# Performance work log

Hardware: AMD Instinct MI355X
Metric: run time of the kernel (lower is better)

Reference implementation:

```python
import jax, jax.numpy as jnp
import numpy as np

N_GRID, N_MESH, N_EDGE, H = 65536, 10242, 131072, 512

def _layernorm(x, g, b, eps=1e-5):
    m = jnp.mean(x, axis=-1, keepdims=True)
    v = jnp.var(x, axis=-1, keepdims=True)
    return (x - m) * jax.lax.rsqrt(v + eps) * g + b

def _mlp(x, W1, b1, W2, b2, g, b):
    # Linear -> SiLU -> Linear -> LayerNorm (GraphCast MeshGraphMLP)
    h = jax.nn.silu(x @ W1 + b1)
    return _layernorm(h @ W2 + b2, g, b)

def setup_inputs() -> dict:
    key = jax.random.key(0)
    ks = jax.random.split(key, 16)
    s = lambda fan_in: 1.0 / np.sqrt(fan_in)
    inp = {
        'grid_node_features': jax.random.normal(ks[0], (N_GRID, H), jnp.float32),
        'mesh_node_features': jax.random.normal(ks[1], (N_MESH, H), jnp.float32),
        'grid2mesh_edge_features': jax.random.normal(ks[2], (N_EDGE, H), jnp.float32),
        'src_indices': jax.random.randint(ks[3], (N_EDGE,), 0, N_GRID),
        'dst_indices': jax.random.randint(ks[4], (N_EDGE,), 0, N_MESH),
        # edge MLP: in = concat(edge, src, dst) = 3H
        'We1': jax.random.normal(ks[5], (3 * H, H), jnp.float32) * s(3 * H),
        'be1': jnp.zeros((H,), jnp.float32),
        'We2': jax.random.normal(ks[6], (H, H), jnp.float32) * s(H),
        'be2': jnp.zeros((H,), jnp.float32),
        'ge': jnp.ones((H,), jnp.float32), 'bbe': jnp.zeros((H,), jnp.float32),
        # node MLP: in = concat(node, agg) = 2H
        'Wn1': jax.random.normal(ks[7], (2 * H, H), jnp.float32) * s(2 * H),
        'bn1': jnp.zeros((H,), jnp.float32),
        'Wn2': jax.random.normal(ks[8], (H, H), jnp.float32) * s(H),
        'bn2': jnp.zeros((H,), jnp.float32),
        'gn': jnp.ones((H,), jnp.float32), 'bbn': jnp.zeros((H,), jnp.float32),
        # grid node MLP: H -> H
        'Wg1': jax.random.normal(ks[9], (H, H), jnp.float32) * s(H),
        'bg1': jnp.zeros((H,), jnp.float32),
        'Wg2': jax.random.normal(ks[10], (H, H), jnp.float32) * s(H),
        'bg2': jnp.zeros((H,), jnp.float32),
        'gg': jnp.ones((H,), jnp.float32), 'bbg': jnp.zeros((H,), jnp.float32),
    }
    return inp

def reference(grid_node_features, mesh_node_features, grid2mesh_edge_features,
              src_indices, dst_indices,
              We1, be1, We2, be2, ge, bbe,
              Wn1, bn1, Wn2, bn2, gn, bbn,
              Wg1, bg1, Wg2, bg2, gg, bbg):
    # --- MeshEdgeBlock: gather src/dst, concat, MLP, residual on edges ---
    cat_e = jnp.concatenate([grid2mesh_edge_features,
                             grid_node_features[src_indices],
                             mesh_node_features[dst_indices]], axis=-1)  # [E, 3H]
    e_feats = grid2mesh_edge_features + _mlp(cat_e, We1, be1, We2, be2, ge, bbe)
    # --- MeshNodeBlock: scatter-sum edges to mesh nodes, concat, MLP ---
    agg = jax.ops.segment_sum(e_feats, dst_indices, num_segments=N_MESH)  # [M, H]
    cat_n = jnp.concatenate([mesh_node_features, agg], axis=-1)  # [M, 2H]
    n_feats = _mlp(cat_n, Wn1, bn1, Wn2, bn2, gn, bbn)
    mesh_out = mesh_node_features + n_feats
    # --- grid node MLP + residual ---
    grid_out = grid_node_features + _mlp(grid_node_features, Wg1, bg1, Wg2, bg2, gg, bbg)
    return (grid_out, mesh_out)
```

## Files before the change

### kernel.cpp

```cpp
#include <hip/hip_runtime.h>
#include <stdint.h>

typedef unsigned short u16;
typedef unsigned int   u32;
typedef unsigned char  u8;

using bf16x8 = __attribute__((ext_vector_type(8))) short;
using f32x4  = __attribute__((ext_vector_type(4))) float;

#define DEVF static __device__ __forceinline__

DEVF u16 f2bf(float f){
  u32 u = __builtin_bit_cast(u32, f);
  u32 r = u + 0x7FFFu + ((u >> 16) & 1u);
  return (u16)(r >> 16);
}
DEVF float bf2f(u16 h){
  u32 u = ((u32)h) << 16;
  return __builtin_bit_cast(float, u);
}

DEVF void gload_lds16(const u16* g, u16* s){
  __builtin_amdgcn_global_load_lds(
      (const __attribute__((address_space(1))) u32*)g,
      (__attribute__((address_space(3))) u32*)(u32)(uintptr_t)s,
      16, 0, 0);
}


__global__ __launch_bounds__(256) void k_f32_to_bf16(const float* __restrict__ in,
                                                     u16* __restrict__ out, long n){
  long i = (long)blockIdx.x * blockDim.x + threadIdx.x;
  long stride = (long)gridDim.x * blockDim.x;
  for (long j = i * 8; j < n; j += stride * 8){
    float4 a = *(const float4*)(in + j);
    float4 b = *(const float4*)(in + j + 4);
    bf16x8 v;
    v[0]=(short)f2bf(a.x); v[1]=(short)f2bf(a.y); v[2]=(short)f2bf(a.z); v[3]=(short)f2bf(a.w);
    v[4]=(short)f2bf(b.x); v[5]=(short)f2bf(b.y); v[6]=(short)f2bf(b.z); v[7]=(short)f2bf(b.w);
    *(bf16x8*)(out + j) = v;
  }
}

__global__ __launch_bounds__(256)
void k_conv_perm(const float* __restrict__ in, const int* __restrict__ pos,
                 u16* __restrict__ out, int E){
  int e = blockIdx.x * 4 + (threadIdx.x >> 6);
  int l = threadIdx.x & 63;
  if (e >= E) return;
  const float* r = in + (size_t)e * 512 + l * 8;
  float4 a = *(const float4*)r, b = *(const float4*)(r + 4);
  bf16x8 v;
  v[0]=(short)f2bf(a.x); v[1]=(short)f2bf(a.y); v[2]=(short)f2bf(a.z); v[3]=(short)f2bf(a.w);
  v[4]=(short)f2bf(b.x); v[5]=(short)f2bf(b.y); v[6]=(short)f2bf(b.z); v[7]=(short)f2bf(b.w);
  *(bf16x8*)(out + (size_t)pos[e] * 512 + l * 8) = v;
}

__global__ __launch_bounds__(256) void k_zero_i32(int* __restrict__ p, int n){
  int i = blockIdx.x * 256 + threadIdx.x;
  if (i < n) p[i] = 0;
}

__global__ __launch_bounds__(256) void k_transpose_w_off(const float* __restrict__ W,
                                                         u16* __restrict__ Wt,
                                                         int K, int N, int k0){
  int idx = blockIdx.x * 256 + threadIdx.x;
  if (idx < K * N){
    int k = idx / N, n = idx - k * N;
    Wt[(size_t)n * K + k] = f2bf(W[(size_t)(k + k0) * N + n]);
  }
}


__global__ __launch_bounds__(256)
void k_hist(const int* __restrict__ key, int* __restrict__ cnt, int E){
  int e = blockIdx.x * 256 + threadIdx.x;
  if (e < E) atomicAdd(&cnt[key[e]], 1);
}

__global__ __launch_bounds__(1024)
void k_scan(const int* __restrict__ cnt, int* __restrict__ offs, int n){
  __shared__ int part[1024];
  int t = threadIdx.x;
  const int PER = (n + 1023) / 1024;
  int base = t * PER;
  int s = 0;
  for (int i = 0; i < PER; ++i){ int idx = base + i; if (idx < n) s += cnt[idx]; }
  part[t] = s;
  __syncthreads();
  for (int o = 1; o < 1024; o <<= 1){
    int v = (t >= o) ? part[t - o] : 0;
    __syncthreads();
    part[t] += v;
    __syncthreads();
  }
  int run = (t == 0) ? 0 : part[t - 1];
  for (int i = 0; i < PER; ++i){
    int idx = base + i;
    if (idx < n){ offs[idx] = run; run += cnt[idx]; }
  }
  if (t == 1023) offs[n] = part[1023];
}

__global__ __launch_bounds__(256)
void k_scatter_pos(const int* __restrict__ key, const int* __restrict__ srcIn,
                   const int* __restrict__ offs, int* __restrict__ cur,
                   int* __restrict__ pos, int* __restrict__ srcD,
                   int* __restrict__ dstD, int E){
  int e = blockIdx.x * 256 + threadIdx.x;
  if (e < E){
    int d = key[e];
    int p = offs[d] + atomicAdd(&cur[d], 1);
    pos[e] = p;
    srcD[p] = srcIn[e];
    dstD[p] = d;
  }
}


#define LDA4(BUF, MH, KK, AF) \
  _Pragma("unroll") for (int m_ = 0; m_ < 4; ++m_) \
    AF[m_] = *(const bf16x8*)&lA[BUF][(wm * 128 + (MH) * 64 + m_ * 16 + lane16) * 64 + \
                                      ((((KK) << 2) | kl) ^ (lane16 & 7)) * 8];

#define LDB4(BUF, KK, BFR) \
  _Pragma("unroll") for (int n_ = 0; n_ < 4; ++n_) \
    BFR[n_] = *(const bf16x8*)&lB[BUF][(wn * 64 + n_ * 16 + lane16) * 64 + \
                                       ((((KK) << 2) | kl) ^ (lane16 & 7)) * 8];

#define PHASE_MFMA(MH, AF, BFR) \
  __builtin_amdgcn_s_setprio(1); \
  _Pragma("unroll") for (int m_ = 0; m_ < 4; ++m_) \
    _Pragma("unroll") for (int n_ = 0; n_ < 4; ++n_) \
      acc[(MH) * 4 + m_][n_] = __builtin_amdgcn_mfma_f32_16x16x32_bf16( \
          AF[m_], BFR[n_], acc[(MH) * 4 + m_][n_], 0, 0, 0); \
  __builtin_amdgcn_s_setprio(0);

#define STAGE_A(BUF, KT_, RND) do{ \
    const int k0_ = (KT_) * 64; \
    const u16* ga_; \
    if (MODE == 0){ ga_ = A + (size_t)srows[RND] * K + k0_ + kchunk; } \
    else { \
      int seg_ = k0_ >> 9, klo_ = k0_ & 511; \
      const u16* b_ = (seg_ == 0) ? A  + (size_t)srows[RND] * 512 \
                                  : G1 + (size_t)sidx1[RND] * 512; \
      ga_ = b_ + klo_ + kchunk; \
    } \
    gload_lds16(ga_, &lA[BUF][((RND) * 64 + w * 8) * 64]); \
  }while(0)

#define STAGE_B(BUF, KT_, RND) \
  gload_lds16(bptr[RND] + (KT_) * 64 + kchunk, &lB[BUF][((RND) * 64 + w * 8) * 64])

#define STAGE8(BUF, KT_) do{ \
    STAGE_A(BUF, KT_, 0); STAGE_A(BUF, KT_, 1); STAGE_A(BUF, KT_, 2); STAGE_A(BUF, KT_, 3); \
    STAGE_B(BUF, KT_, 0); STAGE_B(BUF, KT_, 1); STAGE_B(BUF, KT_, 2); STAGE_B(BUF, KT_, 3); \
  }while(0)

#define WAITBAR(N) do{ \
    asm volatile("s_waitcnt vmcnt(" #N ")" ::: "memory"); \
    __builtin_amdgcn_s_barrier(); \
    __builtin_amdgcn_sched_barrier(0); \
  }while(0)

template<int MODE, int EPI>
__global__ __launch_bounds__(512)
void k_gemm256(const u16* __restrict__ A, const u16* __restrict__ G1, const u16* __restrict__ G2,
               const int* __restrict__ srcI, const int* __restrict__ dstI,
               const u16* __restrict__ Bt, const float* __restrict__ bias,
               void* __restrict__ out, int M, int K)
{
  __shared__ __align__(16) u16 lA[2][256 * 64];
  __shared__ __align__(16) u16 lB[2][256 * 64];

  const int tid = threadIdx.x;
  const int w = tid >> 6, l = tid & 63;

  const int nwg = gridDim.x * gridDim.y;
  const int wgf = blockIdx.y * gridDim.x + blockIdx.x;
  const int lg  = (wgf & 7) * (nwg >> 3) + (wgf >> 3);
  const int col0 = (lg % gridDim.x) * 256;
  const int row0 = (lg / gridDim.x) * 256;

  int srows[4], sidx1[4];
  const u16* bptr[4];
  #pragma unroll
  for (int it = 0; it < 4; ++it){
    int r = row0 + it * 64 + w * 8 + (l >> 3);
    if (r >= M) r = M - 1;
    srows[it] = r;
    if (MODE == 1){ sidx1[it] = srcI[r]; }
    int n = col0 + it * 64 + w * 8 + (l >> 3);
    bptr[it] = Bt + (size_t)n * K;
  }
  const int kchunk = ((l & 7) ^ (l >> 3)) * 8;

  f32x4 acc[8][4];
  #pragma unroll
  for (int m = 0; m < 8; ++m)
    #pragma unroll
    for (int n = 0; n < 4; ++n)
      acc[m][n] = (f32x4){0.f, 0.f, 0.f, 0.f};

  const int wm = w >> 2, wn = w & 3;
  const int lane16 = l & 15, kl = l >> 4;

  const int KT = K >> 6;

  STAGE8(0, 0);

  for (int kt = 0; kt < KT; ++kt){
    const int buf = kt & 1;

    WAITBAR(0);

    if (kt + 1 < KT){ STAGE8(buf ^ 1, kt + 1); }
    __builtin_amdgcn_sched_barrier(0);

    bf16x8 af[4], bfr[4];
    LDB4(buf, 0, bfr);
    LDA4(buf, 0, 0, af);
    PHASE_MFMA(0, af, bfr);

    LDA4(buf, 1, 0, af);
    PHASE_MFMA(1, af, bfr);

    LDB4(buf, 1, bfr);
    LDA4(buf, 0, 1, af);
    PHASE_MFMA(0, af, bfr);

    LDA4(buf, 1, 1, af);
    PHASE_MFMA(1, af, bfr);
  }

  #pragma unroll
  for (int m = 0; m < 8; ++m){
    int rbase = row0 + wm * 128 + m * 16 + kl * 4;
    #pragma unroll
    for (int j = 0; j < 4; ++j){
      int rg = rbase + j;
      if (rg < M){
        int dd = 0;
        if (EPI == 3) dd = dstI[rg];
        #pragma unroll
        for (int n = 0; n < 4; ++n){
          int cg = col0 + wn * 64 + n * 16 + lane16;
          float v = acc[m][n][j];
          if (EPI == 0){
            v += bias[cg];
            v = v / (1.f + __expf(-v));
            ((u16*)out)[(size_t)rg * 512 + cg] = f2bf(v);
          } else if (EPI == 3){
            v += bias[cg] + bf2f(G2[(size_t)dd * 512 + cg]);
            v = v / (1.f + __expf(-v));
            ((u16*)out)[(size_t)rg * 512 + cg] = f2bf(v);
          } else if (EPI == 1){
            ((u16*)out)[(size_t)rg * 512 + cg] = f2bf(v);
          } else {
            ((float*)out)[(size_t)rg * 512 + cg] = v;
          }
        }
      }
    }
  }
}


template<int MODE, int EPI>
__global__ __launch_bounds__(256)
void k_gemm(const u16* __restrict__ A, const u16* __restrict__ G1, const u16* __restrict__ G2,
            const int* __restrict__ src, const int* __restrict__ dst,
            const u16* __restrict__ Bt, const float* __restrict__ bias,
            void* __restrict__ out, int M, int K)
{
  __shared__ __align__(16) u16 lA[128 * 64];
  __shared__ __align__(16) u16 lB[128 * 64];

  const int tid = threadIdx.x;
  const int w = tid >> 6, l = tid & 63;
  const int row0 = blockIdx.x * 128;
  const int col0 = blockIdx.y * 128;

  int srows[4];
  const u16* bptr[4];
  #pragma unroll
  for (int it = 0; it < 4; ++it){
    int r = row0 + it * 32 + w * 8 + (l >> 3);
    if (r >= M) r = M - 1;
    srows[it] = r;
    int n = col0 + it * 32 + w * 8 + (l >> 3);
    bptr[it] = Bt + (size_t)n * K;
  }
  const int kchunk = (l & 7) * 8;

  f32x4 acc[4][4];
  #pragma unroll
  for (int m = 0; m < 4; ++m)
    #pragma unroll
    for (int n = 0; n < 4; ++n)
      acc[m][n] = (f32x4){0.f, 0.f, 0.f, 0.f};

  const int wm = w >> 1, wn = w & 1;
  const int lane16 = l & 15, kl = l >> 4;

  const int KT = K >> 6;
  for (int kt = 0; kt < KT; ++kt){
    const int k0 = kt * 64;
    __syncthreads();
    #pragma unroll
    for (int it = 0; it < 4; ++it){
      const u16* ga;
      if (MODE == 0){
        ga = A + (size_t)srows[it] * K + k0 + kchunk;
      } else {
        int seg = k0 >> 9, klocal = k0 & 511;
        const u16* base = (seg == 0) ? A  + (size_t)srows[it] * 512
                                     : G1 + (size_t)srows[it] * 512;
        ga = base + klocal + kchunk;
      }
      gload_lds16(ga, &lA[(it * 32 + w * 8) * 64]);
      gload_lds16(bptr[it] + k0 + kchunk, &lB[(it * 32 + w * 8) * 64]);
    }
    __syncthreads();

    #pragma unroll
    for (int kk = 0; kk < 2; ++kk){
      bf16x8 af[4], bfr[4];
      #pragma unroll
      for (int m = 0; m < 4; ++m)
        af[m] = *(const bf16x8*)&lA[(wm * 64 + m * 16 + lane16) * 64 + kk * 32 + kl * 8];
      #pragma unroll
      for (int n = 0; n < 4; ++n)
        bfr[n] = *(const bf16x8*)&lB[(wn * 64 + n * 16 + lane16) * 64 + kk * 32 + kl * 8];
      #pragma unroll
      for (int m = 0; m < 4; ++m)
        #pragma unroll
        for (int n = 0; n < 4; ++n)
          acc[m][n] = __builtin_amdgcn_mfma_f32_16x16x32_bf16(af[m], bfr[n], acc[m][n], 0, 0, 0);
    }
  }

  #pragma unroll
  for (int m = 0; m < 4; ++m){
    int rbase = row0 + wm * 64 + m * 16 + kl * 4;
    #pragma unroll
    for (int n = 0; n < 4; ++n){
      int cg = col0 + wn * 64 + n * 16 + lane16;
      #pragma unroll
      for (int j = 0; j < 4; ++j){
        int rg = rbase + j;
        if (rg < M){
          float v = acc[m][n][j];
          if (EPI == 0){
            v += bias[cg];
            v = v / (1.f + __expf(-v));
            ((u16*)out)[(size_t)rg * 512 + cg] = f2bf(v);
          } else if (EPI == 1){
            ((u16*)out)[(size_t)rg * 512 + cg] = f2bf(v);
          } else {
            ((float*)out)[(size_t)rg * 512 + cg] = v;
          }
        }
      }
    }
  }
}


__global__ __launch_bounds__(256)
void k_agg(const u16* __restrict__ e2, const float* __restrict__ be2,
           const float* __restrict__ ge, const float* __restrict__ bbe,
           const u16* __restrict__ ebf, const int* __restrict__ offs,
           u16* __restrict__ aggbf, int Mn)
{
  int node = blockIdx.x * 4 + (threadIdx.x >> 6);
  int l = threadIdx.x & 63;
  if (node >= Mn) return;
  int p0 = offs[node], p1 = offs[node + 1];

  float b2c[8], gc[8], bbc[8];
  #pragma unroll
  for (int j = 0; j < 8; ++j){
    int c = l * 8 + j;
    b2c[j] = be2[c]; gc[j] = ge[c]; bbc[j] = bbe[c];
  }

  float acc[8] = {0.f,0.f,0.f,0.f,0.f,0.f,0.f,0.f};
  for (int p = p0; p < p1; ++p){
    bf16x8 v  = *(const bf16x8*)(e2  + (size_t)p * 512 + l * 8);
    bf16x8 rv = *(const bf16x8*)(ebf + (size_t)p * 512 + l * 8);
    float x[8], s = 0.f, sq = 0.f;
    #pragma unroll
    for (int j = 0; j < 8; ++j){
      x[j] = bf2f((u16)v[j]) + b2c[j];
      s += x[j]; sq += x[j] * x[j];
    }
    #pragma unroll
    for (int o = 32; o; o >>= 1){ s += __shfl_xor(s, o); sq += __shfl_xor(sq, o); }
    float mean = s * (1.f / 512.f);
    float var = sq * (1.f / 512.f) - mean * mean;
    float rs = rsqrtf(var + 1e-5f);
    #pragma unroll
    for (int j = 0; j < 8; ++j)
      acc[j] += (x[j] - mean) * rs * gc[j] + bbc[j] + bf2f((u16)rv[j]);
  }

  bf16x8 o8;
  #pragma unroll
  for (int j = 0; j < 8; ++j) o8[j] = (short)f2bf(acc[j]);
  *(bf16x8*)(aggbf + (size_t)node * 512 + l * 8) = o8;
}


__global__ __launch_bounds__(256)
void k_ln_out(const float* __restrict__ x2, const float* __restrict__ b2,
              const float* __restrict__ g, const float* __restrict__ bb,
              const float* __restrict__ resid, float* __restrict__ out, int R)
{
  int row = blockIdx.x * 4 + (threadIdx.x >> 6);
  int l = threadIdx.x & 63;
  if (row >= R) return;
  const float* xr = x2 + (size_t)row * 512 + l * 8;
  float4 a = *(const float4*)xr, b4 = *(const float4*)(xr + 4);
  float x[8] = {a.x, a.y, a.z, a.w, b4.x, b4.y, b4.z, b4.w};
  float s = 0.f, sq = 0.f;
  #pragma unroll
  for (int j = 0; j < 8; ++j){
    x[j] += b2[l * 8 + j];
    s += x[j]; sq += x[j] * x[j];
  }
  #pragma unroll
  for (int o = 32; o; o >>= 1){ s += __shfl_xor(s, o); sq += __shfl_xor(sq, o); }
  float mean = s * (1.f / 512.f);
  float var = sq * (1.f / 512.f) - mean * mean;
  float rs = rsqrtf(var + 1e-5f);
  const float* rr = resid + (size_t)row * 512 + l * 8;
  float* po = out + (size_t)row * 512 + l * 8;
  #pragma unroll
  for (int j = 0; j < 8; ++j){
    int c = l * 8 + j;
    po[j] = (x[j] - mean) * rs * g[c] + bb[c] + rr[j];
  }
}

__global__ __launch_bounds__(256)
void k_ln_out_bb(const u16* __restrict__ x2, const float* __restrict__ b2,
                 const float* __restrict__ g, const float* __restrict__ bb,
                 const u16* __restrict__ resid, float* __restrict__ out, int R)
{
  int row = blockIdx.x * 4 + (threadIdx.x >> 6);
  int l = threadIdx.x & 63;
  if (row >= R) return;
  bf16x8 xv = *(const bf16x8*)(x2 + (size_t)row * 512 + l * 8);
  float x[8], s = 0.f, sq = 0.f;
  #pragma unroll
  for (int j = 0; j < 8; ++j){
    x[j] = bf2f((u16)xv[j]) + b2[l * 8 + j];
    s += x[j]; sq += x[j] * x[j];
  }
  #pragma unroll
  for (int o = 32; o; o >>= 1){ s += __shfl_xor(s, o); sq += __shfl_xor(sq, o); }
  float mean = s * (1.f / 512.f);
  float var = sq * (1.f / 512.f) - mean * mean;
  float rs = rsqrtf(var + 1e-5f);
  bf16x8 rv = *(const bf16x8*)(resid + (size_t)row * 512 + l * 8);
  float* po = out + (size_t)row * 512 + l * 8;
  #pragma unroll
  for (int j = 0; j < 8; ++j){
    int c = l * 8 + j;
    po[j] = (x[j] - mean) * rs * g[c] + bb[c] + bf2f((u16)rv[j]);
  }
}


extern "C" void kernel_launch(void* const* d_in, const int* in_sizes, int n_in,
                              void* d_out, int out_size, void* d_ws, size_t ws_size,
                              hipStream_t stream)
{
  const int N_GRID = 65536, N_MESH = 10242, N_EDGE = 131072, H = 512;

  const float* grid_f = (const float*)d_in[0];
  const float* mesh_f = (const float*)d_in[1];
  const float* edge_f = (const float*)d_in[2];
  const int*   src    = (const int*)d_in[3];
  const int*   dst    = (const int*)d_in[4];
  const float* We1 = (const float*)d_in[5];  const float* be1 = (const float*)d_in[6];
  const float* We2 = (const float*)d_in[7];  const float* be2 = (const float*)d_in[8];
  const float* ge  = (const float*)d_in[9];  const float* bbe = (const float*)d_in[10];
  const float* Wn1 = (const float*)d_in[11]; const float* bn1 = (const float*)d_in[12];
  const float* Wn2 = (const float*)d_in[13]; const float* bn2 = (const float*)d_in[14];
  const float* gn  = (const float*)d_in[15]; const float* bbn = (const float*)d_in[16];
  const float* Wg1 = (const float*)d_in[17]; const float* bg1 = (const float*)d_in[18];
  const float* Wg2 = (const float*)d_in[19]; const float* bg2 = (const float*)d_in[20];
  const float* gg  = (const float*)d_in[21]; const float* bbg = (const float*)d_in[22];

  u8* ws = (u8*)d_ws;
  const size_t MiB = 1u << 20;
  u16*  Gbf   = (u16*)(ws + 0);
  u16*  Mbf   = (u16*)(ws + 64  * MiB);
  u16*  AggBf = (u16*)(ws + 75  * MiB);
  u16*  We1t  = (u16*)(ws + 86  * MiB);
  u16*  Wpm   = (u16*)(ws + 86  * MiB + 1048576);
  u16*  We2t  = (u16*)(ws + 86  * MiB + 1572864);
  u16*  Wn1t  = (u16*)(ws + 86  * MiB + 2097152);
  u16*  Wn2t  = (u16*)(ws + 86  * MiB + 3145728);
  u16*  Wg1t  = (u16*)(ws + 86  * MiB + 3670016);
  u16*  Wg2t  = (u16*)(ws + 86  * MiB + 4194304);
  int*  offs_d = (int*)(ws + 91 * MiB);
  int*  cnt_d  = (int*)(ws + 91 * MiB) + 10496;
  int*  cur_d  = (int*)(ws + 91 * MiB) + 20992;
  int*  pos_d  = (int*)(ws + 92 * MiB);
  int*  srcD   = (int*)(ws + 92 * MiB) + 131072;
  int*  dstD   = (int*)(ws + 92 * MiB) + 262144;
  u16*  Pm    = (u16*)(ws + 96 * MiB);
  u16*  He    = (u16*)(ws + 112 * MiB);
  u8*   Big   =  ws + 240 * MiB;
  u16*  Ebf   = (u16*)Big;
  float* N2   = (float*)Big;
  u16*  G2    = (u16*)Big;

  float* grid_out = (float*)d_out;
  float* mesh_out = (float*)d_out + (size_t)N_GRID * H;
  u16*  E2    = (u16*)d_out;

  k_zero_i32<<<(20992 + 255) / 256, 256, 0, stream>>>(cnt_d, 20992);
  k_hist<<<N_EDGE / 256, 256, 0, stream>>>(dst, cnt_d, N_EDGE);
  k_scan<<<1, 1024, 0, stream>>>(cnt_d, offs_d, N_MESH);
  k_scatter_pos<<<N_EDGE / 256, 256, 0, stream>>>(dst, src, offs_d, cur_d, pos_d, srcD, dstD, N_EDGE);

  k_f32_to_bf16<<<2048, 256, 0, stream>>>(grid_f, Gbf, (long)N_GRID * H);
  k_f32_to_bf16<<<1024, 256, 0, stream>>>(mesh_f, Mbf, (long)N_MESH * H);
  k_conv_perm<<<N_EDGE / 4, 256, 0, stream>>>(edge_f, pos_d, Ebf, N_EDGE);
  k_transpose_w_off<<<(1024 * 512 + 255) / 256, 256, 0, stream>>>(We1, We1t, 1024, 512, 0);
  k_transpose_w_off<<<(512  * 512 + 255) / 256, 256, 0, stream>>>(We1, Wpm, 512, 512, 1024);
  k_transpose_w_off<<<(512  * 512 + 255) / 256, 256, 0, stream>>>(We2, We2t, 512, 512, 0);
  k_transpose_w_off<<<(1024 * 512 + 255) / 256, 256, 0, stream>>>(Wn1, Wn1t, 1024, 512, 0);
  k_transpose_w_off<<<(512  * 512 + 255) / 256, 256, 0, stream>>>(Wn2, Wn2t, 512, 512, 0);
  k_transpose_w_off<<<(512  * 512 + 255) / 256, 256, 0, stream>>>(Wg1, Wg1t, 512, 512, 0);
  k_transpose_w_off<<<(512  * 512 + 255) / 256, 256, 0, stream>>>(Wg2, Wg2t, 512, 512, 0);

  dim3 gpm((N_MESH + 127) / 128, 4);
  k_gemm<0, 1><<<gpm, 256, 0, stream>>>(Mbf, nullptr, nullptr, nullptr, nullptr, Wpm, nullptr, Pm, N_MESH, 512);

  dim3 ge1(2, N_EDGE / 256);
  k_gemm256<1, 3><<<ge1, 512, 0, stream>>>(Ebf, Gbf, Pm, srcD, dstD, We1t, be1, He, N_EDGE, 1024);
  k_gemm256<0, 1><<<ge1, 512, 0, stream>>>(He, nullptr, nullptr, nullptr, nullptr, We2t, nullptr, E2, N_EDGE, 512);
  k_agg<<<(N_MESH + 3) / 4, 256, 0, stream>>>(E2, be2, ge, bbe, Ebf, offs_d, AggBf, N_MESH);

  dim3 gn1((N_MESH + 127) / 128, 4);
  k_gemm<1, 0><<<gn1, 256, 0, stream>>>(Mbf, AggBf, nullptr, nullptr, nullptr, Wn1t, bn1, He, N_MESH, 1024);
  k_gemm<0, 2><<<gn1, 256, 0, stream>>>(He, nullptr, nullptr, nullptr, nullptr, Wn2t, nullptr, N2, N_MESH, 512);
  k_ln_out<<<(N_MESH + 3) / 4, 256, 0, stream>>>(N2, bn2, gn, bbn, mesh_f, mesh_out, N_MESH);

  dim3 gg1(2, N_GRID / 256);
  k_gemm256<0, 0><<<gg1, 512, 0, stream>>>(Gbf, nullptr, nullptr, nullptr, nullptr, Wg1t, bg1, He, N_GRID, 512);
  k_gemm256<0, 1><<<gg1, 512, 0, stream>>>(He, nullptr, nullptr, nullptr, nullptr, Wg2t, nullptr, G2, N_GRID, 512);
  k_ln_out_bb<<<N_GRID / 4, 256, 0, stream>>>(G2, bg2, gg, bbg, Gbf, grid_out, N_GRID);
}
```

Before: 899.9 us.

## Split GEMM LDS tiles into k-halves and interleave staging with MFMA phases

Reorganizes the 256x256 GEMM's LDS buffers into two 32-wide k-halves per stage, with a matching swizzle and load mapping. Next-tile global-to-LDS loads are issued in four slices interleaved with the MFMA phases, using partial vmcnt waits and a mid-iteration barrier. The goal is to overlap global fetch latency with compute instead of issuing all loads at the top of each iteration. The cost is an extra barrier and explicit lgkmcnt waits per iteration, and the correctness of the waits depends on vmcnt counting exactly four loads per slice. The small GEMM's shared arrays are renamed to avoid clashes.

```diff
diff --git a/kernel.cpp b/kernel.cpp
--- a/kernel.cpp
+++ b/kernel.cpp
@@ -120,13 +120,13 @@
 
 #define LDA4(BUF, MH, KK, AF) \
   _Pragma("unroll") for (int m_ = 0; m_ < 4; ++m_) \
-    AF[m_] = *(const bf16x8*)&lA[BUF][(wm * 128 + (MH) * 64 + m_ * 16 + lane16) * 64 + \
-                                      ((((KK) << 2) | kl) ^ (lane16 & 7)) * 8];
+    AF[m_] = *(const bf16x8*)&lA[BUF][KK][(wm * 128 + (MH) * 64 + m_ * 16 + lane16) * 32 + \
+                                          (kl ^ ((lane16 >> 1) & 3)) * 8];
 
 #define LDB4(BUF, KK, BFR) \
   _Pragma("unroll") for (int n_ = 0; n_ < 4; ++n_) \
-    BFR[n_] = *(const bf16x8*)&lB[BUF][(wn * 64 + n_ * 16 + lane16) * 64 + \
-                                       ((((KK) << 2) | kl) ^ (lane16 & 7)) * 8];
+    BFR[n_] = *(const bf16x8*)&lB[BUF][KK][(wn * 64 + n_ * 16 + lane16) * 32 + \
+                                           (kl ^ ((lane16 >> 1) & 3)) * 8];
 
 #define PHASE_MFMA(MH, AF, BFR) \
   __builtin_amdgcn_s_setprio(1); \
@@ -136,30 +136,31 @@
           AF[m_], BFR[n_], acc[(MH) * 4 + m_][n_], 0, 0, 0); \
   __builtin_amdgcn_s_setprio(0);
 
-#define STAGE_A(BUF, KT_, RND) do{ \
-    const int k0_ = (KT_) * 64; \
+#define STAGE_A(BUF, KT_, HH, PP) do{ \
+    const int k0_ = (KT_) * 64 + (HH) * 32; \
     const u16* ga_; \
-    if (MODE == 0){ ga_ = A + (size_t)srows[RND] * K + k0_ + kchunk; } \
+    if (MODE == 0){ ga_ = A + (size_t)srows[PP] * K + k0_ + kchunk; } \
     else { \
       int seg_ = k0_ >> 9, klo_ = k0_ & 511; \
-      const u16* b_ = (seg_ == 0) ? A  + (size_t)srows[RND] * 512 \
-                                  : G1 + (size_t)sidx1[RND] * 512; \
+      const u16* b_ = (seg_ == 0) ? A  + (size_t)srows[PP] * 512 \
+                                  : G1 + (size_t)sidx1[PP] * 512; \
       ga_ = b_ + klo_ + kchunk; \
     } \
-    gload_lds16(ga_, &lA[BUF][((RND) * 64 + w * 8) * 64]); \
+    gload_lds16(ga_, &lA[BUF][HH][((PP) * 128 + w * 16) * 32]); \
   }while(0)
 
-#define STAGE_B(BUF, KT_, RND) \
-  gload_lds16(bptr[RND] + (KT_) * 64 + kchunk, &lB[BUF][((RND) * 64 + w * 8) * 64])
-
-#define STAGE8(BUF, KT_) do{ \
-    STAGE_A(BUF, KT_, 0); STAGE_A(BUF, KT_, 1); STAGE_A(BUF, KT_, 2); STAGE_A(BUF, KT_, 3); \
-    STAGE_B(BUF, KT_, 0); STAGE_B(BUF, KT_, 1); STAGE_B(BUF, KT_, 2); STAGE_B(BUF, KT_, 3); \
-  }while(0)
+#define STAGE_B(BUF, KT_, HH, PP) \
+  gload_lds16(bptr[PP] + (KT_) * 64 + (HH) * 32 + kchunk, \
+              &lB[BUF][HH][((PP) * 128 + w * 16) * 32])
 
 #define WAITBAR(N) do{ \
     asm volatile("s_waitcnt vmcnt(" #N ")" ::: "memory"); \
     __builtin_amdgcn_s_barrier(); \
+    __builtin_amdgcn_sched_barrier(0); \
+  }while(0)
+
+#define LGK0 do{ \
+    asm volatile("s_waitcnt lgkmcnt(0)" ::: "memory"); \
     __builtin_amdgcn_sched_barrier(0); \
   }while(0)
 
@@ -170,8 +171,8 @@
                const u16* __restrict__ Bt, const float* __restrict__ bias,
                void* __restrict__ out, int M, int K)
 {
-  __shared__ __align__(16) u16 lA[2][256 * 64];
-  __shared__ __align__(16) u16 lB[2][256 * 64];
+  __shared__ __align__(16) u16 lA[2][2][256 * 32];
+  __shared__ __align__(16) u16 lB[2][2][256 * 32];
 
   const int tid = threadIdx.x;
   const int w = tid >> 6, l = tid & 63;
@@ -182,18 +183,18 @@
   const int col0 = (lg % gridDim.x) * 256;
   const int row0 = (lg / gridDim.x) * 256;
 
-  int srows[4], sidx1[4];
-  const u16* bptr[4];
-  #pragma unroll
-  for (int it = 0; it < 4; ++it){
-    int r = row0 + it * 64 + w * 8 + (l >> 3);
+  int srows[2], sidx1[2];
+  const u16* bptr[2];
+  #pragma unroll
+  for (int it = 0; it < 2; ++it){
+    int r = row0 + it * 128 + w * 16 + (l >> 2);
     if (r >= M) r = M - 1;
     srows[it] = r;
     if (MODE == 1){ sidx1[it] = srcI[r]; }
-    int n = col0 + it * 64 + w * 8 + (l >> 3);
+    int n = col0 + it * 128 + w * 16 + (l >> 2);
     bptr[it] = Bt + (size_t)n * K;
   }
-  const int kchunk = ((l & 7) ^ (l >> 3)) * 8;
+  const int kchunk = ((l & 3) ^ ((l >> 3) & 3)) * 8;
 
   f32x4 acc[8][4];
   #pragma unroll
@@ -207,29 +208,38 @@
 
   const int KT = K >> 6;
 
-  STAGE8(0, 0);
+  STAGE_A(0, 0, 0, 0); STAGE_A(0, 0, 0, 1); STAGE_B(0, 0, 0, 0); STAGE_B(0, 0, 0, 1);
+  STAGE_A(0, 0, 1, 0); STAGE_A(0, 0, 1, 1); STAGE_B(0, 0, 1, 0); STAGE_B(0, 0, 1, 1);
 
   for (int kt = 0; kt < KT; ++kt){
     const int buf = kt & 1;
-
-    WAITBAR(0);
-
-    if (kt + 1 < KT){ STAGE8(buf ^ 1, kt + 1); }
-    __builtin_amdgcn_sched_barrier(0);
-
+    const bool more = (kt + 1 < KT);
     bf16x8 af[4], bfr[4];
+
+    WAITBAR(4);
+
+    if (more){ STAGE_A(buf ^ 1, kt + 1, 0, 0); STAGE_A(buf ^ 1, kt + 1, 0, 1); }
     LDB4(buf, 0, bfr);
     LDA4(buf, 0, 0, af);
+    LGK0;
     PHASE_MFMA(0, af, bfr);
 
+    if (more){ STAGE_B(buf ^ 1, kt + 1, 0, 0); STAGE_B(buf ^ 1, kt + 1, 0, 1); }
     LDA4(buf, 1, 0, af);
+    LGK0;
     PHASE_MFMA(1, af, bfr);
 
+    if (more){ WAITBAR(4); } else { WAITBAR(0); }
+
+    if (more){ STAGE_A(buf ^ 1, kt + 1, 1, 0); STAGE_A(buf ^ 1, kt + 1, 1, 1); }
     LDB4(buf, 1, bfr);
     LDA4(buf, 0, 1, af);
+    LGK0;
     PHASE_MFMA(0, af, bfr);
 
+    if (more){ STAGE_B(buf ^ 1, kt + 1, 1, 0); STAGE_B(buf ^ 1, kt + 1, 1, 1); }
     LDA4(buf, 1, 1, af);
+    LGK0;
     PHASE_MFMA(1, af, bfr);
   }
 
@@ -273,8 +283,8 @@
             const u16* __restrict__ Bt, const float* __restrict__ bias,
             void* __restrict__ out, int M, int K)
 {
-  __shared__ __align__(16) u16 lA[128 * 64];
-  __shared__ __align__(16) u16 lB[128 * 64];
+  __shared__ __align__(16) u16 lAx[128 * 64];
+  __shared__ __align__(16) u16 lBx[128 * 64];
 
   const int tid = threadIdx.x;
   const int w = tid >> 6, l = tid & 63;
@@ -318,8 +328,8 @@
                                      : G1 + (size_t)srows[it] * 512;
         ga = base + klocal + kchunk;
       }
-      gload_lds16(ga, &lA[(it * 32 + w * 8) * 64]);
-      gload_lds16(bptr[it] + k0 + kchunk, &lB[(it * 32 + w * 8) * 64]);
+      gload_lds16(ga, &lAx[(it * 32 + w * 8) * 64]);
+      gload_lds16(bptr[it] + k0 + kchunk, &lBx[(it * 32 + w * 8) * 64]);
     }
     __syncthreads();
 
@@ -328,10 +338,10 @@
       bf16x8 af[4], bfr[4];
       #pragma unroll
       for (int m = 0; m < 4; ++m)
-        af[m] = *(const bf16x8*)&lA[(wm * 64 + m * 16 + lane16) * 64 + kk * 32 + kl * 8];
+        af[m] = *(const bf16x8*)&lAx[(wm * 64 + m * 16 + lane16) * 64 + kk * 32 + kl * 8];
       #pragma unroll
       for (int n = 0; n < 4; ++n)
-        bfr[n] = *(const bf16x8*)&lB[(wn * 64 + n * 16 + lane16) * 64 + kk * 32 + kl * 8];
+        bfr[n] = *(const bf16x8*)&lBx[(wn * 64 + n * 16 + lane16) * 64 + kk * 32 + kl * 8];
       #pragma unroll
       for (int m = 0; m < 4; ++m)
         #pragma unroll
```

Result: slower. 929.7 us (+3.3%).
